# Kernel optimization log

Measured on AMD Instinct MI355X. Metric: run time of the kernel, lower is better.

The kernel has to match this reference:

```python
import jax, jax.numpy as jnp
import numpy as np

GATE_SLOPE = 10.0
ALPHA = 0.8


def setup_inputs() -> dict:
    key = jax.random.key(0)
    k0, k1, k2, k3, k4, k5 = jax.random.split(key, 6)
    B, I, O, NB = 512, 128, 64, 8
    x = jax.random.normal(k0, (B, I), dtype=jnp.float32)
    k = jax.random.uniform(k1, (I, O, NB), dtype=jnp.float32) * 2.0 + 0.5
    Ec = jax.random.uniform(k2, (I, O, NB), dtype=jnp.float32) * 2.0 + 0.5
    Ps = jax.random.uniform(k3, (I, O, NB), dtype=jnp.float32) * 1.5 + 0.5
    bias = jax.random.normal(k4, (I, O, NB), dtype=jnp.float32) * 0.1
    coef = jax.random.normal(k5, (I, O, NB), dtype=jnp.float32)
    return {"x": x, "k": k, "Ec": Ec, "Ps": Ps, "bias": bias, "coef": coef}


def reference(x, k, Ec, Ps, bias, coef):
    # x: [B, I]; params: [I, O, NB]
    xe = x[:, :, None, None]  # [B, I, 1, 1], broadcasts against [I, O, NB]
    # The torch loop writes prev_x = x_sample each iteration, so sample b sees
    # x[b-1] as prev (x[-1] = 0 from the initial buffer). branch_sign is never
    # written back, so branch_snap == 1 always. prev is detached in torch.
    prev = jnp.concatenate([jnp.zeros_like(xe[:1]), xe[:-1]], axis=0)
    prev = jax.lax.stop_gradient(prev)

    is_moving_up = jax.nn.sigmoid(GATE_SLOPE * (xe - prev))          # [B,I,1,1]
    crossed_pos = jax.nn.sigmoid(GATE_SLOPE * (xe - Ec))             # [B,I,O,NB]
    crossed_neg = jax.nn.sigmoid(GATE_SLOPE * (-xe - Ec))            # [B,I,O,NB]
    switch_up = is_moving_up * crossed_pos
    switch_lo = (1.0 - is_moving_up) * crossed_neg
    # target = su*1 + sl*(-1) + (1 - su - sl)*branch_snap, branch_snap = 1
    target = switch_up - switch_lo + (1.0 - switch_up - switch_lo)
    branch_momentum = ALPHA + (1.0 - ALPHA) * target                 # alpha*1 + (1-alpha)*target
    basis = Ps * jnp.tanh(k * (xe + Ec * branch_momentum)) + bias    # [B,I,O,NB]
    return jnp.einsum('bion,ion->bo', basis, coef)                   # sum over (I, NB)
```

## Files before the change

kernel.cpp:

```cpp
#include <hip/hip_runtime.h>


#define GATE_C 14.426950408889634f
#define TANH_C 2.8853900817779268f

constexpr int B = 512, I = 128, O = 64, NB = 8, BT = 16;

__global__ __launch_bounds__(256, 4) void fe_main(
    const float* __restrict__ x, const float* __restrict__ k,
    const float* __restrict__ Ec, const float* __restrict__ Ps,
    const float* __restrict__ bias, const float* __restrict__ coef,
    float* __restrict__ out)
{
  __shared__ float4 p_lds[I * NB];
  __shared__ float2 xc_lds[BT][I + 1];
  __shared__ float red[4];

  const int tid = threadIdx.x;
  const int o  = blockIdx.y;
  const int b0 = blockIdx.x * BT;

  float pbase = 0.f;
  for (int e = tid; e < I * NB; e += 256) {
    const int i = e >> 3, n = e & 7;
    const int g = (i * O + o) * NB + n;
    const float ec = Ec[g], kk = k[g], ps = Ps[g], cf = coef[g], bs = bias[g];
    const float pc = ps * cf;
    p_lds[e] = make_float4(ec, ec * GATE_C, kk * TANH_C, pc);
    pbase += fmaf(bs, cf, pc);
  }

  for (int e = tid; e < BT * I; e += 256) {
    const int bl = e >> 7, i = e & 127;
    const int bg = b0 + bl;
    const float xv = x[bg * I + i];
    const float pv = (bg == 0) ? 0.f : x[(bg - 1) * I + i];
    const float c = -0.4f * __builtin_amdgcn_rcpf(
        1.f + __builtin_amdgcn_exp2f(GATE_C * (xv - pv)));
    xc_lds[bl][i] = make_float2(xv, c);
  }

  #pragma unroll
  for (int m = 1; m < 64; m <<= 1) pbase += __shfl_xor(pbase, m);
  if ((tid & 63) == 0) red[tid >> 6] = pbase;
  __syncthreads();

  const int bl = tid >> 4, ih = (tid >> 3) & 1, n = tid & 7;
  const float4* __restrict__ prow = p_lds + (ih * 64) * 8 + n;
  const float2* __restrict__ xrow = &xc_lds[bl][ih * 64];

  float acc = 0.f;
  #pragma unroll 8
  for (int it = 0; it < 64; ++it) {
    const float2 xc = xrow[it];
    const float4 p  = prow[it * 8];
    const float sg = __builtin_amdgcn_rcpf(
        1.f + __builtin_amdgcn_exp2f(fmaf(xc.x, GATE_C, p.y)));
    const float bm    = fmaf(xc.y, sg, 1.f);
    const float inner = fmaf(p.x, bm, xc.x);
    const float r = __builtin_amdgcn_rcpf(
        1.f + __builtin_amdgcn_exp2f(p.z * inner));
    acc = fmaf(p.w, r, acc);
  }

  acc += __shfl_xor(acc, 1);
  acc += __shfl_xor(acc, 2);
  acc += __shfl_xor(acc, 4);
  acc += __shfl_xor(acc, 8);

  if ((tid & 15) == 0) {
    const float base = red[0] + red[1] + red[2] + red[3];
    out[(b0 + bl) * O + o] = fmaf(-2.f, acc, base);
  }
}

extern "C" void kernel_launch(void* const* d_in, const int* in_sizes, int n_in,
                              void* d_out, int out_size, void* d_ws, size_t ws_size,
                              hipStream_t stream) {
  const float* x    = (const float*)d_in[0];
  const float* k    = (const float*)d_in[1];
  const float* Ec   = (const float*)d_in[2];
  const float* Ps   = (const float*)d_in[3];
  const float* bias = (const float*)d_in[4];
  const float* coef = (const float*)d_in[5];
  float* out = (float*)d_out;

  dim3 grid(B / BT, O);
  fe_main<<<grid, 256, 0, stream>>>(x, k, Ec, Ps, bias, coef, out);
}
```

Measured before the change: 28.19 us.

## Keep per-(i,n) parameters in registers and loop over batch rows

Each thread now owns four (i, n) parameter sets held in registers instead of reading a float4 parameter table from LDS on every iteration. It loops over all 16 batch rows of the tile, broadcasting x values from LDS, and keeps 16 accumulators. A two-stage reduction follows: shuffles inside each lane group, then an LDS exchange with a second sync. The aim is to remove the per-iteration LDS parameter traffic, at the cost of more registers and an extra reduction pass.

```diff
diff --git a/kernel.cpp b/kernel.cpp
--- a/kernel.cpp
+++ b/kernel.cpp
@@ -4,7 +4,7 @@
 #define GATE_C 14.426950408889634f
 #define TANH_C 2.8853900817779268f
 
-constexpr int B = 512, I = 128, O = 64, NB = 8, BT = 16;
+constexpr int B = 512, I = 128, O = 64, NB = 8, BT = 16, NS = 4;
 
 __global__ __launch_bounds__(256, 4) void fe_main(
     const float* __restrict__ x, const float* __restrict__ k,
@@ -12,22 +12,27 @@
     const float* __restrict__ bias, const float* __restrict__ coef,
     float* __restrict__ out)
 {
-  __shared__ float4 p_lds[I * NB];
-  __shared__ float2 xc_lds[BT][I + 1];
+  __shared__ float2 xc[BT][I];
+  __shared__ float racc[BT][33];
   __shared__ float red[4];
 
   const int tid = threadIdx.x;
   const int o  = blockIdx.y;
   const int b0 = blockIdx.x * BT;
+  const int n  = tid & 7;
+  const int i0 = tid >> 3;
 
+  float ec[NS], eg[NS], k2[NS], pc[NS];
   float pbase = 0.f;
-  for (int e = tid; e < I * NB; e += 256) {
-    const int i = e >> 3, n = e & 7;
-    const int g = (i * O + o) * NB + n;
-    const float ec = Ec[g], kk = k[g], ps = Ps[g], cf = coef[g], bs = bias[g];
-    const float pc = ps * cf;
-    p_lds[e] = make_float4(ec, ec * GATE_C, kk * TANH_C, pc);
-    pbase += fmaf(bs, cf, pc);
+  #pragma unroll
+  for (int s = 0; s < NS; ++s) {
+    const int g = ((i0 + 32 * s) * O + o) * NB + n;
+    const float E = Ec[g], K = k[g], P = Ps[g], C = coef[g], Bs = bias[g];
+    ec[s] = E;
+    eg[s] = E * GATE_C;
+    k2[s] = K * TANH_C;
+    pc[s] = P * C;
+    pbase += fmaf(Bs, C, pc[s]);
   }
 
   for (int e = tid; e < BT * I; e += 256) {
@@ -37,7 +42,7 @@
     const float pv = (bg == 0) ? 0.f : x[(bg - 1) * I + i];
     const float c = -0.4f * __builtin_amdgcn_rcpf(
         1.f + __builtin_amdgcn_exp2f(GATE_C * (xv - pv)));
-    xc_lds[bl][i] = make_float2(xv, c);
+    xc[bl][i] = make_float2(xv, c);
   }
 
   #pragma unroll
@@ -45,32 +50,44 @@
   if ((tid & 63) == 0) red[tid >> 6] = pbase;
   __syncthreads();
 
-  const int bl = tid >> 4, ih = (tid >> 3) & 1, n = tid & 7;
-  const float4* __restrict__ prow = p_lds + (ih * 64) * 8 + n;
-  const float2* __restrict__ xrow = &xc_lds[bl][ih * 64];
+  float acc[BT];
+  #pragma unroll
+  for (int bl = 0; bl < BT; ++bl) acc[bl] = 0.f;
 
-  float acc = 0.f;
-  #pragma unroll 8
-  for (int it = 0; it < 64; ++it) {
-    const float2 xc = xrow[it];
-    const float4 p  = prow[it * 8];
-    const float sg = __builtin_amdgcn_rcpf(
-        1.f + __builtin_amdgcn_exp2f(fmaf(xc.x, GATE_C, p.y)));
-    const float bm    = fmaf(xc.y, sg, 1.f);
-    const float inner = fmaf(p.x, bm, xc.x);
-    const float r = __builtin_amdgcn_rcpf(
-        1.f + __builtin_amdgcn_exp2f(p.z * inner));
-    acc = fmaf(p.w, r, acc);
+  #pragma unroll
+  for (int bl = 0; bl < BT; ++bl) {
+    #pragma unroll
+    for (int s = 0; s < NS; ++s) {
+      const float2 v = xc[bl][i0 + 32 * s];
+      const float sg = __builtin_amdgcn_rcpf(
+          1.f + __builtin_amdgcn_exp2f(fmaf(v.x, GATE_C, eg[s])));
+      const float bm    = fmaf(v.y, sg, 1.f);
+      const float inner = fmaf(ec[s], bm, v.x);
+      const float r = __builtin_amdgcn_rcpf(
+          1.f + __builtin_amdgcn_exp2f(k2[s] * inner));
+      acc[bl] = fmaf(pc[s], r, acc[bl]);
+    }
   }
 
-  acc += __shfl_xor(acc, 1);
-  acc += __shfl_xor(acc, 2);
-  acc += __shfl_xor(acc, 4);
-  acc += __shfl_xor(acc, 8);
+  #pragma unroll
+  for (int bl = 0; bl < BT; ++bl) {
+    float a = acc[bl];
+    a += __shfl_xor(a, 1);
+    a += __shfl_xor(a, 2);
+    a += __shfl_xor(a, 4);
+    if (n == 0) racc[bl][i0] = a;
+  }
+  __syncthreads();
 
-  if ((tid & 15) == 0) {
+  const int b = tid >> 4, q = tid & 15;
+  float a = racc[b][q] + racc[b][q + 16];
+  a += __shfl_xor(a, 1);
+  a += __shfl_xor(a, 2);
+  a += __shfl_xor(a, 4);
+  a += __shfl_xor(a, 8);
+  if (q == 0) {
     const float base = red[0] + red[1] + red[2] + red[3];
-    out[(b0 + bl) * O + o] = fmaf(-2.f, acc, base);
+    out[(b0 + b) * O + o] = fmaf(-2.f, a, base);
   }
 }
 
```

New measurement: 39.67 us. +40.7%, slower.

## Use 1024-thread blocks covering 64 batch rows to amortize parameter staging

Applied to the files above, without the earlier changes.

Blocks grow to 1024 threads, and each block handles two tiles of 32 batch rows for one output, so the per-output parameter table staged in LDS is loaded once for 64 rows instead of 16. The grid shrinks from 2048 to 512 blocks. Each thread now covers 32 input features instead of 64, and the cross-lane reduction gains one extra shuffle step. The cost is fewer blocks, which can hurt latency hiding and load balance across CUs, plus an extra barrier per tile.

```diff
diff --git a/kernel.cpp b/kernel.cpp
--- a/kernel.cpp
+++ b/kernel.cpp
@@ -4,9 +4,13 @@
 #define GATE_C 14.426950408889634f
 #define TANH_C 2.8853900817779268f
 
-constexpr int B = 512, I = 128, O = 64, NB = 8, BT = 16;
+constexpr int B = 512, I = 128, O = 64, NB = 8, BT = 32, TILES = 2;
 
-__global__ __launch_bounds__(256, 4) void fe_main(
+__device__ __forceinline__ float sig_neg(float u) {
+  return __builtin_amdgcn_rcpf(1.f + __builtin_amdgcn_exp2f(u));
+}
+
+__global__ __launch_bounds__(1024, 4) void fe_main(
     const float* __restrict__ x, const float* __restrict__ k,
     const float* __restrict__ Ec, const float* __restrict__ Ps,
     const float* __restrict__ bias, const float* __restrict__ coef,
@@ -14,63 +18,68 @@
 {
   __shared__ float4 p_lds[I * NB];
   __shared__ float2 xc_lds[BT][I + 1];
-  __shared__ float red[4];
+  __shared__ float red[16];
 
   const int tid = threadIdx.x;
-  const int o  = blockIdx.y;
-  const int b0 = blockIdx.x * BT;
+  const int o = blockIdx.y;
+  const int bbase = blockIdx.x * (BT * TILES);
 
-  float pbase = 0.f;
-  for (int e = tid; e < I * NB; e += 256) {
-    const int i = e >> 3, n = e & 7;
-    const int g = (i * O + o) * NB + n;
-    const float ec = Ec[g], kk = k[g], ps = Ps[g], cf = coef[g], bs = bias[g];
-    const float pc = ps * cf;
-    p_lds[e] = make_float4(ec, ec * GATE_C, kk * TANH_C, pc);
-    pbase += fmaf(bs, cf, pc);
+  {
+    const int i = tid >> 3, nn = tid & 7;
+    const int g = (i * O + o) * NB + nn;
+    const float E = Ec[g], K = k[g], P = Ps[g], C = coef[g], Bs = bias[g];
+    const float pc = P * C;
+    p_lds[tid] = make_float4(E, E * GATE_C, K * TANH_C, pc);
+    float pbase = fmaf(Bs, C, pc);
+    #pragma unroll
+    for (int m = 1; m < 64; m <<= 1) pbase += __shfl_xor(pbase, m);
+    if ((tid & 63) == 0) red[tid >> 6] = pbase;
   }
 
-  for (int e = tid; e < BT * I; e += 256) {
-    const int bl = e >> 7, i = e & 127;
-    const int bg = b0 + bl;
-    const float xv = x[bg * I + i];
-    const float pv = (bg == 0) ? 0.f : x[(bg - 1) * I + i];
-    const float c = -0.4f * __builtin_amdgcn_rcpf(
-        1.f + __builtin_amdgcn_exp2f(GATE_C * (xv - pv)));
-    xc_lds[bl][i] = make_float2(xv, c);
-  }
+  const int n  = tid & 7;
+  const int ih = (tid >> 3) & 3;
+  const int bl = tid >> 5;
+  const float4* __restrict__ prow = p_lds + (ih * 32) * 8 + n;
 
-  #pragma unroll
-  for (int m = 1; m < 64; m <<= 1) pbase += __shfl_xor(pbase, m);
-  if ((tid & 63) == 0) red[tid >> 6] = pbase;
-  __syncthreads();
+  for (int t = 0; t < TILES; ++t) {
+    const int b0 = bbase + t * BT;
+    __syncthreads();
 
-  const int bl = tid >> 4, ih = (tid >> 3) & 1, n = tid & 7;
-  const float4* __restrict__ prow = p_lds + (ih * 64) * 8 + n;
-  const float2* __restrict__ xrow = &xc_lds[bl][ih * 64];
+    for (int e = tid; e < BT * I; e += 1024) {
+      const int xbl = e >> 7, xi = e & 127;
+      const int bg = b0 + xbl;
+      const float xv = x[bg * I + xi];
+      const float pv = (bg == 0) ? 0.f : x[(bg - 1) * I + xi];
+      const float c = -0.4f * sig_neg(GATE_C * (xv - pv));
+      xc_lds[xbl][xi] = make_float2(xv, c);
+    }
+    __syncthreads();
 
-  float acc = 0.f;
-  #pragma unroll 8
-  for (int it = 0; it < 64; ++it) {
-    const float2 xc = xrow[it];
-    const float4 p  = prow[it * 8];
-    const float sg = __builtin_amdgcn_rcpf(
-        1.f + __builtin_amdgcn_exp2f(fmaf(xc.x, GATE_C, p.y)));
-    const float bm    = fmaf(xc.y, sg, 1.f);
-    const float inner = fmaf(p.x, bm, xc.x);
-    const float r = __builtin_amdgcn_rcpf(
-        1.f + __builtin_amdgcn_exp2f(p.z * inner));
-    acc = fmaf(p.w, r, acc);
-  }
+    const float2* __restrict__ xrow = &xc_lds[bl][ih * 32];
+    float acc = 0.f;
+    #pragma unroll 4
+    for (int it = 0; it < 32; ++it) {
+      const float2 xc = xrow[it];
+      const float4 p  = prow[it * 8];
+      const float sg = sig_neg(fmaf(xc.x, GATE_C, p.y));
+      const float bm = fmaf(xc.y, sg, 1.f);
+      const float inner = fmaf(p.x, bm, xc.x);
+      const float r = sig_neg(p.z * inner);
+      acc = fmaf(p.w, r, acc);
+    }
 
-  acc += __shfl_xor(acc, 1);
-  acc += __shfl_xor(acc, 2);
-  acc += __shfl_xor(acc, 4);
-  acc += __shfl_xor(acc, 8);
+    acc += __shfl_xor(acc, 1);
+    acc += __shfl_xor(acc, 2);
+    acc += __shfl_xor(acc, 4);
+    acc += __shfl_xor(acc, 8);
+    acc += __shfl_xor(acc, 16);
 
-  if ((tid & 15) == 0) {
-    const float base = red[0] + red[1] + red[2] + red[3];
-    out[(b0 + bl) * O + o] = fmaf(-2.f, acc, base);
+    if ((tid & 31) == 0) {
+      float base = 0.f;
+      #pragma unroll
+      for (int w = 0; w < 16; ++w) base += red[w];
+      out[(b0 + bl) * O + o] = fmaf(-2.f, acc, base);
+    }
   }
 }
 
@@ -85,6 +94,6 @@
   const float* coef = (const float*)d_in[5];
   float* out = (float*)d_out;
 
-  dim3 grid(B / BT, O);
-  fe_main<<<grid, 256, 0, stream>>>(x, k, Ec, Ps, bias, coef, out);
+  dim3 grid(B / (BT * TILES), O);
+  fe_main<<<grid, 1024, 0, stream>>>(x, k, Ec, Ps, bias, coef, out);
 }
```

Measured after the change: 25.82 us. -8.4%, faster.
